# Kernel tuning notes

Hardware: AMD Instinct MI355X
Metric: run time of the kernel (lower is better)

The kernel has to match this reference:

```python
import jax, jax.numpy as jnp
import numpy as np

B, T, C, H = 4, 2048, 768, 12
HS = C // H

def setup_inputs() -> dict:
    key = jax.random.key(0)
    ks = jax.random.split(key, 5)
    s = 0.02
    return {
        "x": jax.random.normal(ks[0], (B, T, C), jnp.float32),
        "W_attn": jax.random.normal(ks[1], (C, 3 * C), jnp.float32) * s,
        "b_attn": jnp.zeros((3 * C,), jnp.float32),
        "W_proj": jax.random.normal(ks[2], (C, C), jnp.float32) * s,
        "b_proj": jnp.zeros((C,), jnp.float32),
    }

def reference(x, W_attn, b_attn, W_proj, b_proj):
    Bz, Tz, Cz = x.shape
    qkv = x @ W_attn + b_attn                       # [B,T,3C]
    q, k, v = jnp.split(qkv, 3, axis=-1)
    # [B,T,C] -> [B,H,T,HS]
    def heads(t):
        return t.reshape(Bz, Tz, H, HS).transpose(0, 2, 1, 3)
    q, k, v = heads(q), heads(k), heads(v)
    scale = 1.0 / jnp.sqrt(jnp.asarray(HS, x.dtype))
    att = jnp.einsum("bhqd,bhkd->bhqk", q, k) * scale  # [B,H,T,T]
    causal = jnp.tril(jnp.ones((Tz, Tz), bool))
    att = jnp.where(causal[None, None], att, -jnp.inf)
    att = jax.nn.softmax(att, axis=-1)
    y = jnp.einsum("bhqk,bhkd->bhqd", att, v)       # [B,H,T,HS]
    y = y.transpose(0, 2, 1, 3).reshape(Bz, Tz, Cz)
    return y @ W_proj + b_proj
```

## Files before the change

### kernel.cpp

```cpp
#include <hip/hip_runtime.h>
#include <hip/hip_bf16.h>


typedef short s16x8 __attribute__((ext_vector_type(8)));
typedef float f32x4 __attribute__((ext_vector_type(4)));
typedef unsigned short u16x4 __attribute__((ext_vector_type(4)));
typedef unsigned short u16x8 __attribute__((ext_vector_type(8)));

#define MFMA16 __builtin_amdgcn_mfma_f32_16x16x32_bf16

__device__ __forceinline__ unsigned short f2bf(float f) {
    __hip_bfloat16 h = __float2bfloat16(f);
    return *reinterpret_cast<unsigned short*>(&h);
}

__device__ __forceinline__ void gload16(const unsigned short* g, unsigned short* l) {
    __builtin_amdgcn_global_load_lds(
        (__attribute__((address_space(1))) void*)(const void*)g,
        (__attribute__((address_space(3))) void*)l, 16, 0, 0);
}

__global__ __launch_bounds__(256) void cvt_f32_bf16(
    const float* __restrict__ src, unsigned short* __restrict__ dst, int n4)
{
    int i = blockIdx.x * 256 + threadIdx.x;
    if (i >= n4) return;
    float4 v = reinterpret_cast<const float4*>(src)[i];
    u16x4 o = { f2bf(v.x), f2bf(v.y), f2bf(v.z), f2bf(v.w) };
    reinterpret_cast<u16x4*>(dst)[i] = o;
}

__global__ __launch_bounds__(256) void cvt_transpose(
    const float* __restrict__ src, unsigned short* __restrict__ dst, int R, int C)
{
    __shared__ unsigned short tile[32][33];
    const int c0 = blockIdx.x * 32, r0 = blockIdx.y * 32;
    const int tx = threadIdx.x & 31, ty = threadIdx.x >> 5;
#pragma unroll
    for (int j = 0; j < 32; j += 8)
        tile[ty + j][tx] = f2bf(src[(size_t)(r0 + ty + j) * C + c0 + tx]);
    __syncthreads();
#pragma unroll
    for (int j = 0; j < 32; j += 8)
        dst[(size_t)(c0 + ty + j) * R + r0 + tx] = tile[tx][ty + j];
}

template<bool SCALEQ, bool OUT_BF16>
__global__ __launch_bounds__(256, 2) void gemm_bt(
    const unsigned short* __restrict__ A, const unsigned short* __restrict__ Bt,
    const float* __restrict__ bias, void* __restrict__ Cout,
    int M, int N, int K)
{
    __shared__ unsigned short lds_a[128 * 64];
    __shared__ unsigned short lds_b[128 * 64];

    const int tid = threadIdx.x, lane = tid & 63, w = tid >> 6;
    const int wr = w >> 1, wc = w & 1;
    const int lr = lane & 15, lg = lane >> 4;

    const int nbx = gridDim.x;
    const int bid = blockIdx.x + nbx * blockIdx.y;
    const int cpx = (nbx * gridDim.y) >> 3;
    const int swz = (bid & 7) * cpx + (bid >> 3);
    const int m0 = (swz / nbx) * 128, n0 = (swz % nbx) * 128;

    f32x4 acc[4][4];
#pragma unroll
    for (int mi = 0; mi < 4; ++mi)
#pragma unroll
        for (int ni = 0; ni < 4; ++ni)
            acc[mi][ni] = f32x4{0.f, 0.f, 0.f, 0.f};

    const int srow = 8 * w + (lane >> 3);
    const int sslot = ((lane & 7) ^ (lane >> 3)) * 8;
    const unsigned short* Ap = A  + (size_t)(m0 + srow) * K + sslot;
    const unsigned short* Bp = Bt + (size_t)(n0 + srow) * K + sslot;
    unsigned short* la = lds_a + w * 512;
    unsigned short* lb = lds_b + w * 512;

    for (int k0 = 0; k0 < K; k0 += 64) {
#pragma unroll
        for (int p = 0; p < 4; ++p) {
            gload16(Ap + (size_t)(32 * p) * K + k0, la + 2048 * p);
            gload16(Bp + (size_t)(32 * p) * K + k0, lb + 2048 * p);
        }
        __syncthreads();

#pragma unroll
        for (int kh = 0; kh < 2; ++kh) {
            s16x8 af[4], bfr[4];
#pragma unroll
            for (int mi = 0; mi < 4; ++mi) {
                const int row = wr * 64 + mi * 16 + lr;
                af[mi] = *reinterpret_cast<const s16x8*>(
                    &lds_a[row * 64 + ((kh * 32 + lg * 8) ^ ((row & 7) << 3))]);
            }
#pragma unroll
            for (int ni = 0; ni < 4; ++ni) {
                const int row = wc * 64 + ni * 16 + lr;
                bfr[ni] = *reinterpret_cast<const s16x8*>(
                    &lds_b[row * 64 + ((kh * 32 + lg * 8) ^ ((row & 7) << 3))]);
            }
#pragma unroll
            for (int mi = 0; mi < 4; ++mi)
#pragma unroll
                for (int ni = 0; ni < 4; ++ni)
                    acc[mi][ni] = MFMA16(af[mi], bfr[ni], acc[mi][ni], 0, 0, 0);
        }
        __syncthreads();
    }

#pragma unroll
    for (int ni = 0; ni < 4; ++ni) {
        int col = n0 + wc * 64 + ni * 16 + lr;
        float bs = bias[col];
        float scq = (SCALEQ && col < 768) ? 0.18033688011112042f : 1.0f;
#pragma unroll
        for (int mi = 0; mi < 4; ++mi)
#pragma unroll
            for (int r = 0; r < 4; ++r) {
                int row = m0 + wr * 64 + mi * 16 + lg * 4 + r;
                float v = (acc[mi][ni][r] + bs) * scq;
                if (OUT_BF16)
                    ((unsigned short*)Cout)[(size_t)row * N + col] = f2bf(v);
                else
                    ((float*)Cout)[(size_t)row * N + col] = v;
            }
    }
}

__global__ __launch_bounds__(256, 3) void gemm_bt64(
    const unsigned short* __restrict__ A, const unsigned short* __restrict__ Bt,
    const float* __restrict__ bias, float* __restrict__ Cout,
    int M, int N, int K)
{
    __shared__ unsigned short lds_a[128 * 64];
    __shared__ unsigned short lds_b[64 * 64];

    const int tid = threadIdx.x, lane = tid & 63, w = tid >> 6;
    const int lr = lane & 15, lg = lane >> 4;

    const int nbx = gridDim.x;
    const int bid = blockIdx.x + nbx * blockIdx.y;
    const int cpx = (nbx * gridDim.y) >> 3;
    const int swz = (bid & 7) * cpx + (bid >> 3);
    const int m0 = (swz / nbx) * 128, n0 = (swz % nbx) * 64;

    f32x4 acc[2][4];
#pragma unroll
    for (int mi = 0; mi < 2; ++mi)
#pragma unroll
        for (int ni = 0; ni < 4; ++ni)
            acc[mi][ni] = f32x4{0.f, 0.f, 0.f, 0.f};

    const int srow = 8 * w + (lane >> 3);
    const int sslot = ((lane & 7) ^ (lane >> 3)) * 8;
    const unsigned short* Ap = A  + (size_t)(m0 + srow) * K + sslot;
    const unsigned short* Bp = Bt + (size_t)(n0 + srow) * K + sslot;
    unsigned short* la = lds_a + w * 512;
    unsigned short* lb = lds_b + w * 512;

    for (int k0 = 0; k0 < K; k0 += 64) {
#pragma unroll
        for (int p = 0; p < 4; ++p)
            gload16(Ap + (size_t)(32 * p) * K + k0, la + 2048 * p);
#pragma unroll
        for (int p = 0; p < 2; ++p)
            gload16(Bp + (size_t)(32 * p) * K + k0, lb + 2048 * p);
        __syncthreads();

#pragma unroll
        for (int kh = 0; kh < 2; ++kh) {
            s16x8 af[2], bfr[4];
#pragma unroll
            for (int mi = 0; mi < 2; ++mi) {
                const int row = w * 32 + mi * 16 + lr;
                af[mi] = *reinterpret_cast<const s16x8*>(
                    &lds_a[row * 64 + ((kh * 32 + lg * 8) ^ ((row & 7) << 3))]);
            }
#pragma unroll
            for (int ni = 0; ni < 4; ++ni) {
                const int row = ni * 16 + lr;
                bfr[ni] = *reinterpret_cast<const s16x8*>(
                    &lds_b[row * 64 + ((kh * 32 + lg * 8) ^ ((row & 7) << 3))]);
            }
#pragma unroll
            for (int mi = 0; mi < 2; ++mi)
#pragma unroll
                for (int ni = 0; ni < 4; ++ni)
                    acc[mi][ni] = MFMA16(af[mi], bfr[ni], acc[mi][ni], 0, 0, 0);
        }
        __syncthreads();
    }

#pragma unroll
    for (int ni = 0; ni < 4; ++ni) {
        int col = n0 + ni * 16 + lr;
        float bs = bias[col];
#pragma unroll
        for (int mi = 0; mi < 2; ++mi)
#pragma unroll
            for (int r = 0; r < 4; ++r) {
                int row = m0 + w * 32 + mi * 16 + lg * 4 + r;
                Cout[(size_t)row * N + col] = acc[mi][ni][r] + bs;
            }
    }
}

__global__ __launch_bounds__(256, 4) void attn_fwd(
    const unsigned short* __restrict__ qkv, unsigned short* __restrict__ att)
{
    __shared__ unsigned short lds_k[64 * 72];
    __shared__ unsigned short lds_v[64 * 72 + 64];
    __shared__ unsigned short lds_p[4][32 * 72];

    const int tid = threadIdx.x, lane = tid & 63, w = tid >> 6;
    const int lr = lane & 15, lg = lane >> 4;
    const int bh = blockIdx.x;
    const int qt = 15 - blockIdx.y;
    const int b = bh / 12, h = bh % 12;
    const size_t bT = (size_t)b * 2048;
    const int q0 = qt * 128;
    const int wq = q0 + w * 32;

    s16x8 qf[2][2];
#pragma unroll
    for (int mi = 0; mi < 2; ++mi) {
        const size_t qoff = (bT + wq + mi * 16 + lr) * 2304 + h * 64 + lg * 8;
        qf[mi][0] = *reinterpret_cast<const s16x8*>(qkv + qoff);
        qf[mi][1] = *reinterpret_cast<const s16x8*>(qkv + qoff + 32);
    }

    f32x4 o[2][4];
    f32x4 lsum[2];
#pragma unroll
    for (int mi = 0; mi < 2; ++mi) {
        lsum[mi] = f32x4{0.f, 0.f, 0.f, 0.f};
#pragma unroll
        for (int dt = 0; dt < 4; ++dt) o[mi][dt] = f32x4{0.f, 0.f, 0.f, 0.f};
    }

    const int sr = tid >> 2, sc = (tid & 3) * 16;
    const unsigned short* kbase = qkv + (bT + sr) * 2304 + 768 + h * 64 + sc;
    const unsigned short* vbase = qkv + (bT + sr) * 2304 + 1536 + h * 64 + sc;
    unsigned short* kdst = &lds_k[sr * 72 + sc];
    unsigned short* vdst = &lds_v[sc * 72 + ((sc >> 3) & 7) * 8 + sr];
    const int lrx = lr ^ ((lg & 1) << 3);
    const int nb16 = ((lg >> 1) & 1) << 4;
    const int rsel = ((lr >> 2) & 3) << 3;

    const int nkt = 2 * (qt + 1);

    u16x8 kr0, kr1, vr0, vr1;
    kr0 = *reinterpret_cast<const u16x8*>(kbase);
    kr1 = *reinterpret_cast<const u16x8*>(kbase + 8);
    vr0 = *reinterpret_cast<const u16x8*>(vbase);
    vr1 = *reinterpret_cast<const u16x8*>(vbase + 8);

    for (int kt = 0; kt < nkt; ++kt) {
        const int kv0 = kt * 64;
        *reinterpret_cast<u16x8*>(kdst)     = kr0;
        *reinterpret_cast<u16x8*>(kdst + 8) = kr1;
#pragma unroll
        for (int jj = 0; jj < 8; ++jj)
            vdst[jj * 72 + (jj >> 3) * 8] = vr0[jj];
#pragma unroll
        for (int jj = 8; jj < 16; ++jj)
            vdst[jj * 72 + (jj >> 3) * 8] = vr1[jj - 8];
        __syncthreads();

        {
            const int ktn = (kt + 1 < nkt) ? kt + 1 : kt;
            const size_t off = (size_t)(ktn * 64) * 2304;
            kr0 = *reinterpret_cast<const u16x8*>(kbase + off);
            kr1 = *reinterpret_cast<const u16x8*>(kbase + off + 8);
            vr0 = *reinterpret_cast<const u16x8*>(vbase + off);
            vr1 = *reinterpret_cast<const u16x8*>(vbase + off + 8);
        }

        if (kv0 <= wq + 31) {
            f32x4 sf[2][4];
#pragma unroll
            for (int mi = 0; mi < 2; ++mi)
#pragma unroll
                for (int n = 0; n < 4; ++n) sf[mi][n] = f32x4{0.f, 0.f, 0.f, 0.f};
#pragma unroll
            for (int kk = 0; kk < 2; ++kk)
#pragma unroll
                for (int n = 0; n < 4; ++n) {
                    s16x8 kf = *reinterpret_cast<const s16x8*>(&lds_k[(n * 16 + lr) * 72 + kk * 32 + lg * 8]);
                    sf[0][n] = MFMA16(qf[0][kk], kf, sf[0][n], 0, 0, 0);
                    sf[1][n] = MFMA16(qf[1][kk], kf, sf[1][n], 0, 0, 0);
                }

            if (kv0 + 63 > wq) {
#pragma unroll
                for (int mi = 0; mi < 2; ++mi)
#pragma unroll
                    for (int n = 0; n < 4; ++n)
#pragma unroll
                        for (int r = 0; r < 4; ++r) {
                            int key = kv0 + n * 16 + lr;
                            int row = wq + mi * 16 + lg * 4 + r;
                            if (key > row) sf[mi][n][r] = -1.0e30f;
                        }
            }

#pragma unroll
            for (int mi = 0; mi < 2; ++mi)
#pragma unroll
                for (int n = 0; n < 4; ++n) {
                    f32x4 p;
#pragma unroll
                    for (int r = 0; r < 4; ++r) p[r] = __builtin_amdgcn_exp2f(sf[mi][n][r]);
                    lsum[mi] += p;
                    const int kx = ((n << 4) ^ nb16) + lrx;
#pragma unroll
                    for (int r = 0; r < 4; ++r)
                        lds_p[w][(mi * 16 + lg * 4 + r) * 72 + kx] = f2bf(p[r]);
                }

#pragma unroll
            for (int kk = 0; kk < 2; ++kk) {
                const int pko = (kk * 32 + lg * 8) ^ rsel;
                s16x8 pf0 = *reinterpret_cast<const s16x8*>(&lds_p[w][lr * 72 + pko]);
                s16x8 pf1 = *reinterpret_cast<const s16x8*>(&lds_p[w][(16 + lr) * 72 + pko]);
#pragma unroll
                for (int dt = 0; dt < 4; ++dt) {
                    const int vrow = dt * 16 + lr;
                    s16x8 vf = *reinterpret_cast<const s16x8*>(
                        &lds_v[vrow * 72 + ((vrow >> 3) & 7) * 8 + kk * 32 + lg * 8]);
                    o[0][dt] = MFMA16(pf0, vf, o[0][dt], 0, 0, 0);
                    o[1][dt] = MFMA16(pf1, vf, o[1][dt], 0, 0, 0);
                }
            }
        }
        __syncthreads();
    }

#pragma unroll
    for (int mi = 0; mi < 2; ++mi)
#pragma unroll
        for (int mask = 1; mask < 16; mask <<= 1)
#pragma unroll
            for (int r = 0; r < 4; ++r)
                lsum[mi][r] += __shfl_xor(lsum[mi][r], mask);

#pragma unroll
    for (int mi = 0; mi < 2; ++mi)
#pragma unroll
        for (int dt = 0; dt < 4; ++dt)
#pragma unroll
            for (int r = 0; r < 4; ++r) {
                int qrow = wq + mi * 16 + lg * 4 + r;
                att[(bT + qrow) * 768 + h * 64 + dt * 16 + lr] = f2bf(o[mi][dt][r] / lsum[mi][r]);
            }
}

extern "C" void kernel_launch(void* const* d_in, const int* in_sizes, int n_in,
                              void* d_out, int out_size, void* d_ws, size_t ws_size,
                              hipStream_t stream) {
    const float* x      = (const float*)d_in[0];
    const float* W_attn = (const float*)d_in[1];
    const float* b_attn = (const float*)d_in[2];
    const float* W_proj = (const float*)d_in[3];
    const float* b_proj = (const float*)d_in[4];

    unsigned short* ws    = (unsigned short*)d_ws;
    unsigned short* x_bf  = ws;
    unsigned short* wa_t  = x_bf + 6291456;
    unsigned short* wp_t  = wa_t + 1769472;
    unsigned short* qkv   = wp_t + 589824;
    unsigned short* att   = qkv + 18874368;

    cvt_f32_bf16<<<6144, 256, 0, stream>>>(x, x_bf, 6291456 / 4);
    cvt_transpose<<<dim3(72, 24), 256, 0, stream>>>(W_attn, wa_t, 768, 2304);
    cvt_transpose<<<dim3(24, 24), 256, 0, stream>>>(W_proj, wp_t, 768, 768);

    gemm_bt<true , true ><<<dim3(18, 64), 256, 0, stream>>>(x_bf, wa_t, b_attn, qkv, 8192, 2304, 768);
    attn_fwd<<<dim3(48, 16), 256, 0, stream>>>(qkv, att);
    gemm_bt64<<<dim3(12, 64), 256, 0, stream>>>(att, wp_t, b_proj, (float*)d_out, 8192, 768, 768);
}
```

Baseline: 207.8 us.

## Double-buffer K/V in attention, retile projection GEMM, raise GEMM occupancy

The attention kernel now keeps two K/V LDS buffers, so the next tile is written into the spare buffer while the current one is consumed. This removes one barrier per KV step, but doubles K/V LDS use and lowers the occupancy hint from 4 to 2. The output projection GEMM is retiled from 128x64 to 64x128 blocks, with a 2x2 wave layout, on a 6x128 grid. The QKV GEMM occupancy hint goes from 2 to 3, which may force register spills.

```diff
diff --git a/kernel.cpp b/kernel.cpp
--- a/kernel.cpp
+++ b/kernel.cpp
@@ -46,7 +46,7 @@
 }
 
 template<bool SCALEQ, bool OUT_BF16>
-__global__ __launch_bounds__(256, 2) void gemm_bt(
+__global__ __launch_bounds__(256, 3) void gemm_bt(
     const unsigned short* __restrict__ A, const unsigned short* __restrict__ Bt,
     const float* __restrict__ bias, void* __restrict__ Cout,
     int M, int N, int K)
@@ -129,22 +129,23 @@
     }
 }
 
-__global__ __launch_bounds__(256, 3) void gemm_bt64(
+__global__ __launch_bounds__(256, 3) void gemm_bt_m64(
     const unsigned short* __restrict__ A, const unsigned short* __restrict__ Bt,
     const float* __restrict__ bias, float* __restrict__ Cout,
     int M, int N, int K)
 {
-    __shared__ unsigned short lds_a[128 * 64];
-    __shared__ unsigned short lds_b[64 * 64];
+    __shared__ unsigned short lds_a[64 * 64];
+    __shared__ unsigned short lds_b[128 * 64];
 
     const int tid = threadIdx.x, lane = tid & 63, w = tid >> 6;
+    const int wr = w >> 1, wc = w & 1;
     const int lr = lane & 15, lg = lane >> 4;
 
     const int nbx = gridDim.x;
     const int bid = blockIdx.x + nbx * blockIdx.y;
     const int cpx = (nbx * gridDim.y) >> 3;
     const int swz = (bid & 7) * cpx + (bid >> 3);
-    const int m0 = (swz / nbx) * 128, n0 = (swz % nbx) * 64;
+    const int m0 = (swz / nbx) * 64, n0 = (swz % nbx) * 128;
 
     f32x4 acc[2][4];
 #pragma unroll
@@ -162,10 +163,10 @@
 
     for (int k0 = 0; k0 < K; k0 += 64) {
 #pragma unroll
+        for (int p = 0; p < 2; ++p)
+            gload16(Ap + (size_t)(32 * p) * K + k0, la + 2048 * p);
+#pragma unroll
         for (int p = 0; p < 4; ++p)
-            gload16(Ap + (size_t)(32 * p) * K + k0, la + 2048 * p);
-#pragma unroll
-        for (int p = 0; p < 2; ++p)
             gload16(Bp + (size_t)(32 * p) * K + k0, lb + 2048 * p);
         __syncthreads();
 
@@ -174,13 +175,13 @@
             s16x8 af[2], bfr[4];
 #pragma unroll
             for (int mi = 0; mi < 2; ++mi) {
-                const int row = w * 32 + mi * 16 + lr;
+                const int row = wr * 32 + mi * 16 + lr;
                 af[mi] = *reinterpret_cast<const s16x8*>(
                     &lds_a[row * 64 + ((kh * 32 + lg * 8) ^ ((row & 7) << 3))]);
             }
 #pragma unroll
             for (int ni = 0; ni < 4; ++ni) {
-                const int row = ni * 16 + lr;
+                const int row = wc * 64 + ni * 16 + lr;
                 bfr[ni] = *reinterpret_cast<const s16x8*>(
                     &lds_b[row * 64 + ((kh * 32 + lg * 8) ^ ((row & 7) << 3))]);
             }
@@ -195,23 +196,23 @@
 
 #pragma unroll
     for (int ni = 0; ni < 4; ++ni) {
-        int col = n0 + ni * 16 + lr;
+        int col = n0 + wc * 64 + ni * 16 + lr;
         float bs = bias[col];
 #pragma unroll
         for (int mi = 0; mi < 2; ++mi)
 #pragma unroll
             for (int r = 0; r < 4; ++r) {
-                int row = m0 + w * 32 + mi * 16 + lg * 4 + r;
+                int row = m0 + wr * 32 + mi * 16 + lg * 4 + r;
                 Cout[(size_t)row * N + col] = acc[mi][ni][r] + bs;
             }
     }
 }
 
-__global__ __launch_bounds__(256, 4) void attn_fwd(
+__global__ __launch_bounds__(256, 2) void attn_fwd(
     const unsigned short* __restrict__ qkv, unsigned short* __restrict__ att)
 {
-    __shared__ unsigned short lds_k[64 * 72];
-    __shared__ unsigned short lds_v[64 * 72 + 64];
+    __shared__ unsigned short lds_k[2][64 * 72];
+    __shared__ unsigned short lds_v[2][64 * 72 + 64];
     __shared__ unsigned short lds_p[4][32 * 72];
 
     const int tid = threadIdx.x, lane = tid & 63, w = tid >> 6;
@@ -220,8 +221,7 @@
     const int qt = 15 - blockIdx.y;
     const int b = bh / 12, h = bh % 12;
     const size_t bT = (size_t)b * 2048;
-    const int q0 = qt * 128;
-    const int wq = q0 + w * 32;
+    const int wq = qt * 128 + w * 32;
 
     s16x8 qf[2][2];
 #pragma unroll
@@ -243,35 +243,36 @@
     const int sr = tid >> 2, sc = (tid & 3) * 16;
     const unsigned short* kbase = qkv + (bT + sr) * 2304 + 768 + h * 64 + sc;
     const unsigned short* vbase = qkv + (bT + sr) * 2304 + 1536 + h * 64 + sc;
-    unsigned short* kdst = &lds_k[sr * 72 + sc];
-    unsigned short* vdst = &lds_v[sc * 72 + ((sc >> 3) & 7) * 8 + sr];
+    const int koff = sr * 72 + sc;
+    const int voff = sc * 72 + ((sc >> 3) & 7) * 8 + sr;
     const int lrx = lr ^ ((lg & 1) << 3);
     const int nb16 = ((lg >> 1) & 1) << 4;
     const int rsel = ((lr >> 2) & 3) << 3;
 
     const int nkt = 2 * (qt + 1);
-
-    u16x8 kr0, kr1, vr0, vr1;
-    kr0 = *reinterpret_cast<const u16x8*>(kbase);
-    kr1 = *reinterpret_cast<const u16x8*>(kbase + 8);
-    vr0 = *reinterpret_cast<const u16x8*>(vbase);
-    vr1 = *reinterpret_cast<const u16x8*>(vbase + 8);
+    const size_t TSTEP = (size_t)64 * 2304;
+
+    u16x8 kr0 = *reinterpret_cast<const u16x8*>(kbase);
+    u16x8 kr1 = *reinterpret_cast<const u16x8*>(kbase + 8);
+    u16x8 vr0 = *reinterpret_cast<const u16x8*>(vbase);
+    u16x8 vr1 = *reinterpret_cast<const u16x8*>(vbase + 8);
+    *reinterpret_cast<u16x8*>(&lds_k[0][koff])     = kr0;
+    *reinterpret_cast<u16x8*>(&lds_k[0][koff + 8]) = kr1;
+#pragma unroll
+    for (int jj = 0; jj < 8; ++jj)
+        lds_v[0][voff + jj * 72] = vr0[jj];
+#pragma unroll
+    for (int jj = 8; jj < 16; ++jj)
+        lds_v[0][voff + jj * 72 + 8] = vr1[jj - 8];
+    __syncthreads();
 
     for (int kt = 0; kt < nkt; ++kt) {
+        const int cur = kt & 1;
         const int kv0 = kt * 64;
-        *reinterpret_cast<u16x8*>(kdst)     = kr0;
-        *reinterpret_cast<u16x8*>(kdst + 8) = kr1;
-#pragma unroll
-        for (int jj = 0; jj < 8; ++jj)
-            vdst[jj * 72 + (jj >> 3) * 8] = vr0[jj];
-#pragma unroll
-        for (int jj = 8; jj < 16; ++jj)
-            vdst[jj * 72 + (jj >> 3) * 8] = vr1[jj - 8];
-        __syncthreads();
 
         {
             const int ktn = (kt + 1 < nkt) ? kt + 1 : kt;
-            const size_t off = (size_t)(ktn * 64) * 2304;
+            const size_t off = (size_t)ktn * TSTEP;
             kr0 = *reinterpret_cast<const u16x8*>(kbase + off);
             kr1 = *reinterpret_cast<const u16x8*>(kbase + off + 8);
             vr0 = *reinterpret_cast<const u16x8*>(vbase + off);
@@ -279,6 +280,9 @@
         }
 
         if (kv0 <= wq + 31) {
+            const unsigned short* kb = lds_k[cur];
+            const unsigned short* vb = lds_v[cur];
+
             f32x4 sf[2][4];
 #pragma unroll
             for (int mi = 0; mi < 2; ++mi)
@@ -288,7 +292,8 @@
             for (int kk = 0; kk < 2; ++kk)
 #pragma unroll
                 for (int n = 0; n < 4; ++n) {
-                    s16x8 kf = *reinterpret_cast<const s16x8*>(&lds_k[(n * 16 + lr) * 72 + kk * 32 + lg * 8]);
+                    s16x8 kf = *reinterpret_cast<const s16x8*>(
+                        &kb[(n * 16 + lr) * 72 + kk * 32 + lg * 8]);
                     sf[0][n] = MFMA16(qf[0][kk], kf, sf[0][n], 0, 0, 0);
                     sf[1][n] = MFMA16(qf[1][kk], kf, sf[1][n], 0, 0, 0);
                 }
@@ -329,11 +334,23 @@
                 for (int dt = 0; dt < 4; ++dt) {
                     const int vrow = dt * 16 + lr;
                     s16x8 vf = *reinterpret_cast<const s16x8*>(
-                        &lds_v[vrow * 72 + ((vrow >> 3) & 7) * 8 + kk * 32 + lg * 8]);
+                        &vb[vrow * 72 + ((vrow >> 3) & 7) * 8 + kk * 32 + lg * 8]);
                     o[0][dt] = MFMA16(pf0, vf, o[0][dt], 0, 0, 0);
                     o[1][dt] = MFMA16(pf1, vf, o[1][dt], 0, 0, 0);
                 }
             }
+        }
+
+        {
+            const int nxt = cur ^ 1;
+            *reinterpret_cast<u16x8*>(&lds_k[nxt][koff])     = kr0;
+            *reinterpret_cast<u16x8*>(&lds_k[nxt][koff + 8]) = kr1;
+#pragma unroll
+            for (int jj = 0; jj < 8; ++jj)
+                lds_v[nxt][voff + jj * 72] = vr0[jj];
+#pragma unroll
+            for (int jj = 8; jj < 16; ++jj)
+                lds_v[nxt][voff + jj * 72 + 8] = vr1[jj - 8];
         }
         __syncthreads();
     }
@@ -379,5 +396,5 @@
 
     gemm_bt<true , true ><<<dim3(18, 64), 256, 0, stream>>>(x_bf, wa_t, b_attn, qkv, 8192, 2304, 768);
     attn_fwd<<<dim3(48, 16), 256, 0, stream>>>(qkv, att);
-    gemm_bt64<<<dim3(12, 64), 256, 0, stream>>>(att, wp_t, b_proj, (float*)d_out, 8192, 768, 768);
-}
+    gemm_bt_m64<<<dim3(6, 128), 256, 0, stream>>>(att, wp_t, b_proj, (float*)d_out, 8192, 768, 768);
+}
```

Measured after the change: 196.3 us. 1.06x faster.
